# Performance work log

Hardware: AMD Instinct MI355X
Metric: run time of the kernel (lower is better)

The kernel has to match this reference:

```python
import jax, jax.numpy as jnp
import numpy as np

B, N, D = 4, 4096, 256

def setup_inputs() -> dict:
    key = jax.random.key(0)
    ks = jax.random.split(key, 7)
    def xavier(k, shape):
        fan_in, fan_out = shape[1], shape[0]
        a = jnp.sqrt(6.0 / (fan_in + fan_out))
        return jax.random.uniform(k, shape, jnp.float32, -a, a)
    return {
        "x": jax.random.normal(ks[0], (B, N, D), jnp.float32),
        "Wq": xavier(ks[1], (D, D)),
        "bq": jnp.zeros((D,), jnp.float32),
        "Wk": xavier(ks[2], (D, D)),
        "bk": jnp.zeros((D,), jnp.float32),
        "Wv": xavier(ks[3], (D, D)),
        "bv": jnp.zeros((D,), jnp.float32),
        "scale": jnp.asarray([jnp.sqrt(jnp.float32(D))]),
    }

def reference(x, Wq, bq, Wk, bk, Wv, bv, scale):
    # nn.Linear: y = x @ W.T + b
    q = jnp.einsum('bnd,ed->bne', x, Wq) + bq
    k = jnp.einsum('bnd,ed->bne', x, Wk) + bk
    v = jnp.einsum('bnd,ed->bne', x, Wv) + bv
    scores = jnp.einsum('bqd,bkd->bqk', q, k) / scale[0]  # [B,N,N]
    attn = jax.nn.softmax(scores, axis=-1)
    out = jnp.einsum('bqk,bkd->bqd', attn, v)
    return out
```

## Files before the change

### kernel.cpp

```cpp
#include <hip/hip_runtime.h>
#include <hip/hip_bf16.h>

typedef unsigned int u32;
typedef unsigned short u16;
typedef __attribute__((ext_vector_type(8))) __bf16 bf8v;
typedef __attribute__((ext_vector_type(16))) float f32x16;
typedef __attribute__((ext_vector_type(8))) u16 u16x8;

__device__ inline u16 f2bf(float f) {
    u32 u = __float_as_uint(f);
    u = (u + 0x7FFF + ((u >> 16) & 1)) >> 16;
    return (u16)u;
}
__device__ inline u32 pk2(float a, float b) {
    return (u32)f2bf(a) | ((u32)f2bf(b) << 16);
}
__device__ inline float bf2f(u16 h) { return __uint_as_float(((u32)h) << 16); }

__device__ inline u32 cvtpk(float a, float b) {
    u32 r;
    asm("v_cvt_pk_bf16_f32 %0, %1, %2" : "=v"(r) : "v"(a), "v"(b));
    return r;
}
__device__ inline void plswap(u32& a, u32& b) {
    asm("v_permlane32_swap_b32 %0, %1" : "+v"(a), "+v"(b));
}

__device__ inline void dma16(const u16* g, u16* l) {
    __builtin_amdgcn_global_load_lds(
        (const __attribute__((address_space(1))) void*)g,
        (__attribute__((address_space(3))) void*)l, 16, 0, 0);
}

__global__ void cvt_all(const float* __restrict__ x,
                        const float* __restrict__ wq, const float* __restrict__ wk,
                        const float* __restrict__ wv,
                        u16* __restrict__ xp, u16* __restrict__ wall) {
    const int blk = blockIdx.x;
    if (blk < 2048) {
        int g = blk * 256 + threadIdx.x;
        int row = g >> 5, cp = g & 31;
        const float* s = x + row * 256 + cp * 8;
        float4 a = *(const float4*)s;
        float4 b = *(const float4*)(s + 4);
        uint4 o;
        o.x = pk2(a.x, a.y); o.y = pk2(a.z, a.w);
        o.z = pk2(b.x, b.y); o.w = pk2(b.z, b.w);
        *(uint4*)(xp + (row >> 5) * 8192 + cp * 256 + (row & 31) * 8) = o;
    } else {
        const int bb = blk - 2048;
        const int m = bb >> 5;
        const float* src = m == 0 ? wq : m == 1 ? wk : wv;
        int g = (bb & 31) * 256 + threadIdx.x;
        int row = g >> 5, c = g & 31;
        const float* s = src + row * 256 + c * 8;
        float4 a = *(const float4*)s;
        float4 b = *(const float4*)(s + 4);
        uint4 o;
        o.x = pk2(a.x, a.y); o.y = pk2(a.z, a.w);
        o.z = pk2(b.x, b.y); o.w = pk2(b.z, b.w);
        *(uint4*)(wall + m * 65536 + row * 256 + ((c ^ (row & 7)) * 8)) = o;
    }
}

__global__ __launch_bounds__(256) void qkv_proj(
    const u16* __restrict__ xp, const u16* __restrict__ wall,
    const float* __restrict__ bq, const float* __restrict__ bk, const float* __restrict__ bv,
    const float* __restrict__ scale,
    u16* __restrict__ qp, u16* __restrict__ kp, u16* __restrict__ vp)
{
    __shared__ u16 Ws[128 * 256];

    const int blk = blockIdx.x;
    const int xcd = blk & 7;
    const int r2 = blk >> 3;
    const int rt = r2 / 6;
    const int cz = r2 % 6;
    const int sel = cz >> 1;
    const int colbase = (cz & 1) * 128;
    const int rowbase0 = (xcd * 16 + rt) * 128;

    const float* bias = sel == 0 ? bq : sel == 1 ? bk : bv;
    const float qs = sel == 0 ? 1.44269504088896f / scale[0] : 1.0f;
    const int tid = threadIdx.x;
    const int wave = tid >> 6, lane = tid & 63;
    const int l31 = lane & 31, l5 = lane >> 5;
    const int tg = (rowbase0 >> 5) + wave;

    {
        const u16* wsrc = wall + sel * 65536 + colbase * 256;
#pragma unroll
        for (int j = 0; j < 16; j++) {
            const int i = wave * 16 + j;
            dma16(wsrc + i * 512 + lane * 8, Ws + i * 512);
        }
    }
    asm volatile("s_waitcnt vmcnt(0)" ::: "memory");
    __syncthreads();

    f32x16 acc[4];
#pragma unroll
    for (int cb = 0; cb < 4; cb++)
#pragma unroll
        for (int j = 0; j < 16; j++) acc[cb][j] = 0.f;

    const u16* ap = xp + tg * 8192 + l5 * 256 + l31 * 8;
    const int sw = l31 & 7;
    if (sel < 2) {
#pragma unroll
        for (int kk = 0; kk < 16; kk++) {
            bf8v af = *(const bf8v*)(ap + kk * 512);
            const int co = ((kk * 2 + l5) ^ sw) * 8;
#pragma unroll
            for (int cb = 0; cb < 4; cb++) {
                bf8v bfr = *(const bf8v*)(Ws + (cb * 32 + l31) * 256 + co);
                acc[cb] = __builtin_amdgcn_mfma_f32_32x32x16_bf16(bfr, af, acc[cb], 0, 0, 0);
            }
        }
        u16* base = (sel == 0 ? qp : kp) + tg * 8192;
#pragma unroll
        for (int cb = 0; cb < 4; cb++) {
            const int colb = colbase + cb * 32;
#pragma unroll
            for (int q = 0; q < 4; q++) {
                const float4 b4 = *(const float4*)(bias + colb + 8 * q + 4 * l5);
                const float v0 = (acc[cb][4 * q + 0] + b4.x) * qs;
                const float v1 = (acc[cb][4 * q + 1] + b4.y) * qs;
                const float v2 = (acc[cb][4 * q + 2] + b4.z) * qs;
                const float v3 = (acc[cb][4 * q + 3] + b4.w) * qs;
                uint2 o2 = { cvtpk(v0, v1), cvtpk(v2, v3) };
                *(uint2*)(base + ((colb >> 3) + q) * 256 + l31 * 8 + 4 * l5) = o2;
            }
        }
    } else {
#pragma unroll
        for (int kk = 0; kk < 16; kk++) {
            bf8v af = *(const bf8v*)(ap + kk * 512);
            const int co = ((kk * 2 + l5) ^ sw) * 8;
#pragma unroll
            for (int cb = 0; cb < 4; cb++) {
                bf8v bfr = *(const bf8v*)(Ws + (cb * 32 + l31) * 256 + co);
                acc[cb] = __builtin_amdgcn_mfma_f32_32x32x16_bf16(af, bfr, acc[cb], 0, 0, 0);
            }
        }
        u16* base = vp + tg * 8192;
#pragma unroll
        for (int cb = 0; cb < 4; cb++) {
            const int colb = colbase + cb * 32;
            const float bc = bias[colb + l31];
            const int d0 = colb + l31;
#pragma unroll
            for (int q = 0; q < 4; q++) {
                const float v0 = acc[cb][4 * q + 0] + bc;
                const float v1 = acc[cb][4 * q + 1] + bc;
                const float v2 = acc[cb][4 * q + 2] + bc;
                const float v3 = acc[cb][4 * q + 3] + bc;
                uint2 o2 = { cvtpk(v0, v1), cvtpk(v2, v3) };
                *(uint2*)(base + q * 2048 + d0 * 8 + 4 * l5) = o2;
            }
        }
    }
}

__global__ __launch_bounds__(256, 2) void flash_attn(
    const u16* __restrict__ qp_, const u16* __restrict__ kp_, const u16* __restrict__ vp_,
    u16* __restrict__ Opb, float* __restrict__ ml)
{
    __shared__ u16 Ks[2 * 8192];
    __shared__ u16 Vs[2 * 8192];

    const int tid = threadIdx.x;
    const int wave = tid >> 6, lane = tid & 63;
    const int l31 = lane & 31, l5 = lane >> 5;

    const int blk = blockIdx.x;
    const int slot = blk >> 3;
    const int g = (blk & 7) * 2 + (slot >> 5);
    const int qtile = slot & 31;
    const int b = g >> 2, s = g & 3;
    const int qbase = qtile * 128 + wave * 32;

    bf8v qf[16];
    {
        const u16* qp = qp_ + (b * 128 + qtile * 4 + wave) * 8192 + l31 * 8;
#pragma unroll
        for (int kk = 0; kk < 16; kk++)
            qf[kk] = *(const bf8v*)(qp + (kk * 2 + l5) * 256);
    }

    f32x16 o[8];
#pragma unroll
    for (int i = 0; i < 8; i++)
#pragma unroll
        for (int j = 0; j < 16; j++) o[i][j] = 0.f;
    float lsum = 0.f;

    const u16* kbase = kp_ + (b * 128 + s * 32) * 8192;
    const u16* vbase = vp_ + (b * 128 + s * 32) * 8192;

#pragma unroll
    for (int j = 0; j < 4; j++) {
        const int i = wave * 4 + j;
        dma16(kbase + i * 512 + lane * 8, Ks + i * 512);
    }
#pragma unroll
    for (int j = 0; j < 4; j++) {
        const int i = wave * 4 + j;
        dma16(vbase + i * 512 + lane * 8, Vs + i * 512);
    }
#pragma unroll
    for (int j = 0; j < 4; j++) {
        const int i = wave * 4 + j;
        dma16(kbase + 8192 + i * 512 + lane * 8, Ks + 8192 + i * 512);
    }
    asm volatile("s_waitcnt vmcnt(8)" ::: "memory");
    asm volatile("s_barrier" ::: "memory");

    bf8v pf0, pf1;
    {
        f32x16 c0, c1;
#pragma unroll
        for (int j = 0; j < 16; j++) { c0[j] = 0.f; c1[j] = 0.f; }
#pragma unroll
        for (int j = 0; j < 8; j++) {
            bf8v kf0 = *(const bf8v*)(Ks + (j * 2 + l5) * 256 + l31 * 8);
            c0 = __builtin_amdgcn_mfma_f32_32x32x16_bf16(kf0, qf[j], c0, 0, 0, 0);
            bf8v kf1 = *(const bf8v*)(Ks + ((8 + j) * 2 + l5) * 256 + l31 * 8);
            c1 = __builtin_amdgcn_mfma_f32_32x32x16_bf16(kf1, qf[8 + j], c1, 0, 0, 0);
        }
        float e[16];
#pragma unroll
        for (int r = 0; r < 16; r++)
            e[r] = __builtin_amdgcn_exp2f(c0[r] + c1[r]);
        {
            float s0 = (e[0] + e[1]) + (e[2] + e[3]);
            float s1 = (e[4] + e[5]) + (e[6] + e[7]);
            float s2 = (e[8] + e[9]) + (e[10] + e[11]);
            float s3 = (e[12] + e[13]) + (e[14] + e[15]);
            lsum += (s0 + s1) + (s2 + s3);
        }
        u32 pA = cvtpk(e[0], e[1]), pB = cvtpk(e[2], e[3]);
        u32 pC = cvtpk(e[4], e[5]), pD = cvtpk(e[6], e[7]);
        plswap(pA, pC); plswap(pB, pD);
        u32 pE = cvtpk(e[8], e[9]),  pF = cvtpk(e[10], e[11]);
        u32 pG = cvtpk(e[12], e[13]), pH = cvtpk(e[14], e[15]);
        plswap(pE, pG); plswap(pF, pH);
        union { uint4 u; bf8v v; } u0, u1;
        u0.u = (uint4){pA, pB, pC, pD};
        u1.u = (uint4){pE, pF, pG, pH};
        pf0 = u0.v; pf1 = u1.v;
    }

#pragma unroll 1
    for (int it = 0; it < 31; it++) {
        const int buf = it & 1;
        asm volatile("s_waitcnt vmcnt(0)" ::: "memory");
        asm volatile("s_barrier" ::: "memory");
        {
            const u16* vt_ = vbase + (it + 1) * 8192;
#pragma unroll
            for (int j = 0; j < 4; j++) {
                const int i = wave * 4 + j;
                dma16(vt_ + i * 512 + lane * 8, Vs + (buf ^ 1) * 8192 + i * 512);
            }
            if (it < 30) {
                const u16* kt_ = kbase + (it + 2) * 8192;
#pragma unroll
                for (int j = 0; j < 4; j++) {
                    const int i = wave * 4 + j;
                    dma16(kt_ + i * 512 + lane * 8, Ks + buf * 8192 + i * 512);
                }
            }
        }
        const u16* Kb_ = Ks + (buf ^ 1) * 8192;
        f32x16 c0, c1;
#pragma unroll
        for (int j = 0; j < 16; j++) { c0[j] = 0.f; c1[j] = 0.f; }
#pragma unroll
        for (int j = 0; j < 8; j++) {
            bf8v kf0 = *(const bf8v*)(Kb_ + (j * 2 + l5) * 256 + l31 * 8);
            c0 = __builtin_amdgcn_mfma_f32_32x32x16_bf16(kf0, qf[j], c0, 0, 0, 0);
            bf8v kf1 = *(const bf8v*)(Kb_ + ((8 + j) * 2 + l5) * 256 + l31 * 8);
            c1 = __builtin_amdgcn_mfma_f32_32x32x16_bf16(kf1, qf[8 + j], c1, 0, 0, 0);
        }
        const u16* Vb_ = Vs + buf * 8192;
        float e[16];
#pragma unroll
        for (int j = 0; j < 8; j++) {
            bf8v vf0 = *(const bf8v*)(Vb_ + (l5 * 256 + j * 32 + l31) * 8);
            o[j] = __builtin_amdgcn_mfma_f32_32x32x16_bf16(pf0, vf0, o[j], 0, 0, 0);
            e[2 * j] = __builtin_amdgcn_exp2f(c0[2 * j] + c1[2 * j]);
            bf8v vf1 = *(const bf8v*)(Vb_ + ((2 + l5) * 256 + j * 32 + l31) * 8);
            o[j] = __builtin_amdgcn_mfma_f32_32x32x16_bf16(pf1, vf1, o[j], 0, 0, 0);
            e[2 * j + 1] = __builtin_amdgcn_exp2f(c0[2 * j + 1] + c1[2 * j + 1]);
        }
        {
            float s0 = (e[0] + e[1]) + (e[2] + e[3]);
            float s1 = (e[4] + e[5]) + (e[6] + e[7]);
            float s2 = (e[8] + e[9]) + (e[10] + e[11]);
            float s3 = (e[12] + e[13]) + (e[14] + e[15]);
            lsum += (s0 + s1) + (s2 + s3);
        }
        {
            u32 pA = cvtpk(e[0], e[1]), pB = cvtpk(e[2], e[3]);
            u32 pC = cvtpk(e[4], e[5]), pD = cvtpk(e[6], e[7]);
            plswap(pA, pC); plswap(pB, pD);
            u32 pE = cvtpk(e[8], e[9]),  pF = cvtpk(e[10], e[11]);
            u32 pG = cvtpk(e[12], e[13]), pH = cvtpk(e[14], e[15]);
            plswap(pE, pG); plswap(pF, pH);
            union { uint4 u; bf8v v; } u0, u1;
            u0.u = (uint4){pA, pB, pC, pD};
            u1.u = (uint4){pE, pF, pG, pH};
            pf0 = u0.v; pf1 = u1.v;
        }
    }

    asm volatile("s_waitcnt vmcnt(0)" ::: "memory");
    asm volatile("s_barrier" ::: "memory");
    {
        const u16* Vb_ = Vs + 8192;
#pragma unroll
        for (int j = 0; j < 8; j++) {
            bf8v vf0 = *(const bf8v*)(Vb_ + (l5 * 256 + j * 32 + l31) * 8);
            o[j] = __builtin_amdgcn_mfma_f32_32x32x16_bf16(pf0, vf0, o[j], 0, 0, 0);
            bf8v vf1 = *(const bf8v*)(Vb_ + ((2 + l5) * 256 + j * 32 + l31) * 8);
            o[j] = __builtin_amdgcn_mfma_f32_32x32x16_bf16(pf1, vf1, o[j], 0, 0, 0);
        }
    }

    const int rowg = s * 16384 + b * 4096 + qbase;
    u16* ob = Opb + (size_t)rowg * 256;
#pragma unroll
    for (int nb = 0; nb < 8; nb++)
#pragma unroll
        for (int r = 0; r < 16; r++) {
            const int R = (r & 3) + 8 * (r >> 2) + 4 * l5;
            ob[R * 256 + nb * 32 + l31] = f2bf(o[nb][r]);
        }
    {
        u32 a = __float_as_uint(lsum), b2 = a;
        plswap(a, b2);
        const float tot = lsum + __uint_as_float(l5 ? a : b2);
        if (l5 == 0) ml[rowg + l31] = tot;
    }
}

__global__ __launch_bounds__(256) void combine(
    const u16* __restrict__ Opb, const float* __restrict__ ml, float* __restrict__ out)
{
    const int row = blockIdx.x * 4 + (threadIdx.x >> 6);
    const int lane = threadIdx.x & 63;
    const float denom = ml[row] + ml[16384 + row] + ml[32768 + row] + ml[49152 + row];
    float4 acc = {0.f, 0.f, 0.f, 0.f};
#pragma unroll
    for (int si = 0; si < 4; si++) {
        ushort4 v = *(const ushort4*)(Opb + ((size_t)si * 16384 + row) * 256 + lane * 4);
        acc.x += bf2f(v.x); acc.y += bf2f(v.y);
        acc.z += bf2f(v.z); acc.w += bf2f(v.w);
    }
    const float inv = 1.0f / denom;
    acc.x *= inv; acc.y *= inv; acc.z *= inv; acc.w *= inv;
    *((float4*)(out + (size_t)row * 256) + lane) = acc;
}

extern "C" void kernel_launch(void* const* d_in, const int* in_sizes, int n_in,
                              void* d_out, int out_size, void* d_ws, size_t ws_size,
                              hipStream_t stream) {
    const float* x     = (const float*)d_in[0];
    const float* Wq    = (const float*)d_in[1];
    const float* bq    = (const float*)d_in[2];
    const float* Wk    = (const float*)d_in[3];
    const float* bk    = (const float*)d_in[4];
    const float* Wv    = (const float*)d_in[5];
    const float* bv    = (const float*)d_in[6];
    const float* scale = (const float*)d_in[7];
    float* out = (float*)d_out;

    char* ws = (char*)d_ws;
    u16* xp   = (u16*)ws;
    u16* qp   = (u16*)(ws + (8u  << 20));
    u16* kp   = (u16*)(ws + (16u << 20));
    u16* vp   = (u16*)(ws + (24u << 20));
    u16* wall = (u16*)(ws + (32u << 20));
    u16* Opb  = (u16*)(ws + (34u << 20));
    float* ml = (float*)(ws + (66u << 20));

    cvt_all<<<2144, 256, 0, stream>>>(x, Wq, Wk, Wv, xp, wall);
    qkv_proj<<<768, 256, 0, stream>>>(xp, wall, bq, bk, bv, scale, qp, kp, vp);
    flash_attn<<<512, 256, 0, stream>>>(qp, kp, vp, Opb, ml);
    combine<<<4096, 256, 0, stream>>>(Opb, ml, out);
}
```

Before: 170.6 us.

## Fuse fp32-to-bf16 conversion into QKV projection and raise wave priority around MFMA

Removes the separate cvt_all kernel. The QKV projection now reads fp32 x and weights directly and converts them to bf16 in registers or while staging into shared memory, which saves one launch and the round trip of the bf16 copies through global memory. In exchange, each block now loads fp32 data, twice the bytes, and x is read redundantly by the six column blocks. The weight load becomes synchronous instead of using LDS DMA. It also adds s_setprio around the MFMA/exp sections in flash attention to favour the math waves.

```diff
diff --git a/kernel.cpp b/kernel.cpp
--- a/kernel.cpp
+++ b/kernel.cpp
@@ -12,9 +12,6 @@
     u = (u + 0x7FFF + ((u >> 16) & 1)) >> 16;
     return (u16)u;
 }
-__device__ inline u32 pk2(float a, float b) {
-    return (u32)f2bf(a) | ((u32)f2bf(b) << 16);
-}
 __device__ inline float bf2f(u16 h) { return __uint_as_float(((u32)h) << 16); }
 
 __device__ inline u32 cvtpk(float a, float b) {
@@ -32,40 +29,11 @@
         (__attribute__((address_space(3))) void*)l, 16, 0, 0);
 }
 
-__global__ void cvt_all(const float* __restrict__ x,
-                        const float* __restrict__ wq, const float* __restrict__ wk,
-                        const float* __restrict__ wv,
-                        u16* __restrict__ xp, u16* __restrict__ wall) {
-    const int blk = blockIdx.x;
-    if (blk < 2048) {
-        int g = blk * 256 + threadIdx.x;
-        int row = g >> 5, cp = g & 31;
-        const float* s = x + row * 256 + cp * 8;
-        float4 a = *(const float4*)s;
-        float4 b = *(const float4*)(s + 4);
-        uint4 o;
-        o.x = pk2(a.x, a.y); o.y = pk2(a.z, a.w);
-        o.z = pk2(b.x, b.y); o.w = pk2(b.z, b.w);
-        *(uint4*)(xp + (row >> 5) * 8192 + cp * 256 + (row & 31) * 8) = o;
-    } else {
-        const int bb = blk - 2048;
-        const int m = bb >> 5;
-        const float* src = m == 0 ? wq : m == 1 ? wk : wv;
-        int g = (bb & 31) * 256 + threadIdx.x;
-        int row = g >> 5, c = g & 31;
-        const float* s = src + row * 256 + c * 8;
-        float4 a = *(const float4*)s;
-        float4 b = *(const float4*)(s + 4);
-        uint4 o;
-        o.x = pk2(a.x, a.y); o.y = pk2(a.z, a.w);
-        o.z = pk2(b.x, b.y); o.w = pk2(b.z, b.w);
-        *(uint4*)(wall + m * 65536 + row * 256 + ((c ^ (row & 7)) * 8)) = o;
-    }
-}
-
 __global__ __launch_bounds__(256) void qkv_proj(
-    const u16* __restrict__ xp, const u16* __restrict__ wall,
-    const float* __restrict__ bq, const float* __restrict__ bk, const float* __restrict__ bv,
+    const float* __restrict__ x,
+    const float* __restrict__ wq, const float* __restrict__ bq,
+    const float* __restrict__ wk, const float* __restrict__ bk,
+    const float* __restrict__ wv, const float* __restrict__ bv,
     const float* __restrict__ scale,
     u16* __restrict__ qp, u16* __restrict__ kp, u16* __restrict__ vp)
 {
@@ -80,6 +48,7 @@
     const int colbase = (cz & 1) * 128;
     const int rowbase0 = (xcd * 16 + rt) * 128;
 
+    const float* wsrc = sel == 0 ? wq : sel == 1 ? wk : wv;
     const float* bias = sel == 0 ? bq : sel == 1 ? bk : bv;
     const float qs = sel == 0 ? 1.44269504088896f / scale[0] : 1.0f;
     const int tid = threadIdx.x;
@@ -88,14 +57,19 @@
     const int tg = (rowbase0 >> 5) + wave;
 
     {
-        const u16* wsrc = wall + sel * 65536 + colbase * 256;
 #pragma unroll
         for (int j = 0; j < 16; j++) {
-            const int i = wave * 16 + j;
-            dma16(wsrc + i * 512 + lane * 8, Ws + i * 512);
-        }
-    }
-    asm volatile("s_waitcnt vmcnt(0)" ::: "memory");
+            const int g = j * 256 + tid;
+            const int r = g >> 5, c = g & 31;
+            const float* sp = wsrc + (colbase + r) * 256 + c * 8;
+            float4 a = *(const float4*)sp;
+            float4 b = *(const float4*)(sp + 4);
+            uint4 o;
+            o.x = cvtpk(a.x, a.y); o.y = cvtpk(a.z, a.w);
+            o.z = cvtpk(b.x, b.y); o.w = cvtpk(b.z, b.w);
+            *(uint4*)(Ws + r * 256 + ((c ^ (r & 7)) * 8)) = o;
+        }
+    }
     __syncthreads();
 
     f32x16 acc[4];
@@ -104,12 +78,18 @@
 #pragma unroll
         for (int j = 0; j < 16; j++) acc[cb][j] = 0.f;
 
-    const u16* ap = xp + tg * 8192 + l5 * 256 + l31 * 8;
+    const float* xrow = x + (size_t)(tg * 32 + l31) * 256;
     const int sw = l31 & 7;
     if (sel < 2) {
 #pragma unroll
         for (int kk = 0; kk < 16; kk++) {
-            bf8v af = *(const bf8v*)(ap + kk * 512);
+            const float* sp = xrow + (kk * 2 + l5) * 8;
+            float4 a = *(const float4*)sp;
+            float4 b = *(const float4*)(sp + 4);
+            union { uint4 u; bf8v v; } afu;
+            afu.u.x = cvtpk(a.x, a.y); afu.u.y = cvtpk(a.z, a.w);
+            afu.u.z = cvtpk(b.x, b.y); afu.u.w = cvtpk(b.z, b.w);
+            const bf8v af = afu.v;
             const int co = ((kk * 2 + l5) ^ sw) * 8;
 #pragma unroll
             for (int cb = 0; cb < 4; cb++) {
@@ -135,7 +115,13 @@
     } else {
 #pragma unroll
         for (int kk = 0; kk < 16; kk++) {
-            bf8v af = *(const bf8v*)(ap + kk * 512);
+            const float* sp = xrow + (kk * 2 + l5) * 8;
+            float4 a = *(const float4*)sp;
+            float4 b = *(const float4*)(sp + 4);
+            union { uint4 u; bf8v v; } afu;
+            afu.u.x = cvtpk(a.x, a.y); afu.u.y = cvtpk(a.z, a.w);
+            afu.u.z = cvtpk(b.x, b.y); afu.u.w = cvtpk(b.z, b.w);
+            const bf8v af = afu.v;
             const int co = ((kk * 2 + l5) ^ sw) * 8;
 #pragma unroll
             for (int cb = 0; cb < 4; cb++) {
@@ -272,6 +258,7 @@
                 }
             }
         }
+        __builtin_amdgcn_s_setprio(1);
         const u16* Kb_ = Ks + (buf ^ 1) * 8192;
         f32x16 c0, c1;
 #pragma unroll
@@ -294,6 +281,7 @@
             o[j] = __builtin_amdgcn_mfma_f32_32x32x16_bf16(pf1, vf1, o[j], 0, 0, 0);
             e[2 * j + 1] = __builtin_amdgcn_exp2f(c0[2 * j + 1] + c1[2 * j + 1]);
         }
+        __builtin_amdgcn_s_setprio(0);
         {
             float s0 = (e[0] + e[1]) + (e[2] + e[3]);
             float s1 = (e[4] + e[5]) + (e[6] + e[7]);
@@ -319,6 +307,7 @@
     asm volatile("s_barrier" ::: "memory");
     {
         const u16* Vb_ = Vs + 8192;
+        __builtin_amdgcn_s_setprio(1);
 #pragma unroll
         for (int j = 0; j < 8; j++) {
             bf8v vf0 = *(const bf8v*)(Vb_ + (l5 * 256 + j * 32 + l31) * 8);
@@ -326,6 +315,7 @@
             bf8v vf1 = *(const bf8v*)(Vb_ + ((2 + l5) * 256 + j * 32 + l31) * 8);
             o[j] = __builtin_amdgcn_mfma_f32_32x32x16_bf16(pf1, vf1, o[j], 0, 0, 0);
         }
+        __builtin_amdgcn_s_setprio(0);
     }
 
     const int rowg = s * 16384 + b * 4096 + qbase;
@@ -377,16 +367,13 @@
     float* out = (float*)d_out;
 
     char* ws = (char*)d_ws;
-    u16* xp   = (u16*)ws;
-    u16* qp   = (u16*)(ws + (8u  << 20));
-    u16* kp   = (u16*)(ws + (16u << 20));
-    u16* vp   = (u16*)(ws + (24u << 20));
-    u16* wall = (u16*)(ws + (32u << 20));
-    u16* Opb  = (u16*)(ws + (34u << 20));
-    float* ml = (float*)(ws + (66u << 20));
-
-    cvt_all<<<2144, 256, 0, stream>>>(x, Wq, Wk, Wv, xp, wall);
-    qkv_proj<<<768, 256, 0, stream>>>(xp, wall, bq, bk, bv, scale, qp, kp, vp);
+    u16* qp   = (u16*)ws;
+    u16* kp   = (u16*)(ws + (8u  << 20));
+    u16* vp   = (u16*)(ws + (16u << 20));
+    u16* Opb  = (u16*)(ws + (24u << 20));
+    float* ml = (float*)(ws + (56u << 20));
+
+    qkv_proj<<<768, 256, 0, stream>>>(x, Wq, bq, Wk, bk, Wv, bv, scale, qp, kp, vp);
     flash_attn<<<512, 256, 0, stream>>>(qp, kp, vp, Opb, ml);
     combine<<<4096, 256, 0, stream>>>(Opb, ml, out);
 }
```

Result: no change. 172.8 us (+1.3%).
